# Performance work log

Hardware: AMD Instinct MI355X
Metric: run time of the kernel (lower is better)

Reference implementation:

```python
import jax, jax.numpy as jnp
import numpy as np

NUM_EXPERTS = 8
TOP_K = 2
ROUTE_SCALE = 1.0
DIM = 1024
HID = 1024
B, S = 2, 4096


def setup_inputs() -> dict:
    key = jax.random.key(0)
    ks = jax.random.split(key, 9)
    sc = 0.05
    return {
        "x": jax.random.normal(ks[0], (B, S, DIM), dtype=jnp.float32),
        "gate_w": jax.random.normal(ks[1], (NUM_EXPERTS, DIM), dtype=jnp.float32) * sc,
        "w1": jax.random.normal(ks[2], (NUM_EXPERTS, HID, DIM), dtype=jnp.float32) * sc,
        "w2": jax.random.normal(ks[3], (NUM_EXPERTS, DIM, HID), dtype=jnp.float32) * sc,
        "w3": jax.random.normal(ks[4], (NUM_EXPERTS, HID, DIM), dtype=jnp.float32) * sc,
        "sw1": jax.random.normal(ks[5], (HID, DIM), dtype=jnp.float32) * sc,
        "sw2": jax.random.normal(ks[6], (DIM, HID), dtype=jnp.float32) * sc,
        "sw3": jax.random.normal(ks[7], (HID, DIM), dtype=jnp.float32) * sc,
        "expert_bias": jnp.zeros((NUM_EXPERTS,), dtype=jnp.float32),
    }


def reference(x, gate_w, w1, w2, w3, sw1, sw2, sw3, expert_bias):
    bs, slen, dim = x.shape
    xf = x.reshape(-1, dim)                      # [T, D]

    # ---- router (sigmoid scoring, top-k over scores + bias, gather true scores) ----
    scores = jax.nn.sigmoid((xf @ gate_w.T).astype(jnp.float32))   # [T, E]
    _, sel = jax.lax.top_k(scores + expert_bias[None, :], TOP_K)    # [T, K] int32
    top_scores = jnp.take_along_axis(scores, sel, axis=1) * ROUTE_SCALE  # [T, K]

    # ---- stable sort token-slots by chosen expert (dispatch permutation) ----
    flat_sel = sel.reshape(-1)                       # [T*K]
    order = jnp.argsort(flat_sel, stable=True)       # [T*K]
    scores_sorted = top_scores.reshape(-1)[order]    # [T*K]
    tok_idx = order // TOP_K                         # source token per slot
    expert_ids = flat_sel[order]                     # sorted expert id per slot

    routed = xf[tok_idx]                             # gather [T*K, D]
    # score_before_experts=True: scale inputs by routing score
    routed = (routed.astype(jnp.float32) * scores_sorted[:, None]).astype(x.dtype)

    # ---- grouped expert GLU MLP (loop over fixed expert count, masked) ----
    out_r = jnp.zeros_like(routed)
    for e in range(NUM_EXPERTS):
        m = (expert_ids == e)[:, None]
        h = jax.nn.silu(routed @ w1[e].T) * (routed @ w3[e].T)   # [T*K, H]
        out_r = out_r + jnp.where(m, h @ w2[e].T, jnp.zeros((), routed.dtype))

    # ---- shared expert on all tokens ----
    shared = (jax.nn.silu(xf @ sw1.T) * (xf @ sw3.T)) @ sw2.T    # [T, D]

    # NOTE: original code multiplies by routing scores again after experts
    # (in addition to score_before_experts) -- replicated faithfully.
    out_r = (out_r.astype(jnp.float32) * scores_sorted[:, None]).astype(x.dtype)

    out = shared.at[tok_idx].add(out_r)              # scatter-add combine
    return out.reshape(bs, slen, dim)
```

## Files before the change

### kernel.cpp

```cpp
#include <hip/hip_runtime.h>
#include <stdint.h>

typedef unsigned short u16;
typedef unsigned int u32;

#define T_TOK 8192
#define DIMSZ 1024
#define HIDSZ 1024
#define NE 8
#define NSLOT (T_TOK * 2)
#define NPAD (NSLOT + 1024)

typedef __attribute__((ext_vector_type(8))) __bf16 bf16x8;
typedef __attribute__((ext_vector_type(16))) float f32x16;

#define MFMA32(a, b, c) __builtin_amdgcn_mfma_f32_32x32x16_bf16(a, b, c, 0, 0, 0)

__device__ __forceinline__ size_t ablk(int pos, int c) {
  return ((((size_t)(pos >> 7) * 32 + (c >> 5)) * 4 + ((c >> 3) & 3)) * 128 +
          (pos & 127)) * 8 + (c & 7);
}

__device__ __forceinline__ u16 f2bf(float f) {
  u32 u = __builtin_bit_cast(u32, f);
  u += 0x7FFFu + ((u >> 16) & 1u);
  return (u16)(u >> 16);
}
__device__ __forceinline__ float bflo(u32 v) { return __builtin_bit_cast(float, v << 16); }
__device__ __forceinline__ float bfhi(u32 v) { return __builtin_bit_cast(float, v & 0xffff0000u); }
__device__ __forceinline__ u32 pack2(float a, float b) {
  return (u32)f2bf(a) | ((u32)f2bf(b) << 16);
}
__device__ __forceinline__ float silu_f(float v) { return v / (1.f + expf(-v)); }

__global__ __launch_bounds__(256) void convert_blocked(
    const float* __restrict__ s0, const float* __restrict__ s1,
    const float* __restrict__ s2, const float* __restrict__ ss0,
    const float* __restrict__ ss1, const float* __restrict__ ss2,
    u16* __restrict__ d0, u16* __restrict__ d1, u16* __restrict__ d2,
    u16* __restrict__ ds0, u16* __restrict__ ds1, u16* __restrict__ ds2) {
  __shared__ u16 lt[2048];
  int t = blockIdx.x;
  const float* s;
  u16* d;
  if (t < NE * 16 * 32) {
    s = (blockIdx.y == 0) ? s0 : (blockIdx.y == 1) ? s1 : s2;
    d = (blockIdx.y == 0) ? d0 : (blockIdx.y == 1) ? d1 : d2;
  } else {
    t -= NE * 16 * 32;
    s = (blockIdx.y == 0) ? ss0 : (blockIdx.y == 1) ? ss1 : ss2;
    d = (blockIdx.y == 0) ? ds0 : (blockIdx.y == 1) ? ds1 : ds2;
  }
  int rt = t >> 5, kt = t & 31;
  const float* sp = s + (size_t)rt * 64 * 1024 + kt * 32;
  int nl = threadIdx.x >> 2, k0 = (threadIdx.x & 3) * 8;
  float4 a = *(const float4*)(sp + (size_t)nl * 1024 + k0);
  float4 b = *(const float4*)(sp + (size_t)nl * 1024 + k0 + 4);
  uint4 p;
  p.x = pack2(a.x, a.y); p.y = pack2(a.z, a.w);
  p.z = pack2(b.x, b.y); p.w = pack2(b.z, b.w);
  *(uint4*)&lt[(threadIdx.x & 3) * 512 + nl * 8] = p;
  __syncthreads();
  *(uint4*)(d + (size_t)t * 2048 + threadIdx.x * 8) = *(const uint4*)&lt[threadIdx.x * 8];
}

__global__ __launch_bounds__(256) void router_kernel(
    const float* __restrict__ x, const float* __restrict__ gw,
    const float* __restrict__ bias, int* __restrict__ sel,
    float* __restrict__ selscore, u16* __restrict__ xb) {
  int t = blockIdx.x * 4 + (threadIdx.x >> 6);
  int lane = threadIdx.x & 63;
  float a[NE];
#pragma unroll
  for (int e = 0; e < NE; e++) a[e] = 0.f;
#pragma unroll
  for (int j = 0; j < 4; j++) {
    int c = j * 256 + lane * 4;
    float4 xv = *(const float4*)&x[(size_t)t * DIMSZ + c];
    uint2 p;
    p.x = pack2(xv.x, xv.y);
    p.y = pack2(xv.z, xv.w);
    *(uint2*)&xb[ablk(t, c)] = p;
#pragma unroll
    for (int e = 0; e < NE; e++) {
      float4 gv = *(const float4*)&gw[e * DIMSZ + c];
      a[e] = fmaf(xv.x, gv.x, fmaf(xv.y, gv.y, fmaf(xv.z, gv.z, fmaf(xv.w, gv.w, a[e]))));
    }
  }
#pragma unroll
  for (int off = 1; off < 64; off <<= 1)
#pragma unroll
    for (int e = 0; e < NE; e++) a[e] += __shfl_xor(a[e], off);
  if (lane == 0) {
    float s[NE], b[NE];
#pragma unroll
    for (int e = 0; e < NE; e++) {
      s[e] = 1.f / (1.f + expf(-a[e]));
      b[e] = s[e] + bias[e];
    }
    int e1 = 0; float v1 = b[0];
#pragma unroll
    for (int e = 1; e < NE; e++) if (b[e] > v1) { v1 = b[e]; e1 = e; }
    int e2 = -1; float v2 = -1e30f;
#pragma unroll
    for (int e = 0; e < NE; e++) if (e != e1 && b[e] > v2) { v2 = b[e]; e2 = e; }
    sel[t * 2] = e1; sel[t * 2 + 1] = e2;
    selscore[t * 2] = s[e1];
    selscore[t * 2 + 1] = s[e2];
  }
}

__global__ __launch_bounds__(1024) void rank_kernel(
    const int* __restrict__ sel, const float* __restrict__ selscore,
    int* __restrict__ slot2pos, float* __restrict__ slot_score,
    int* __restrict__ counts, int* __restrict__ offsets) {
  __shared__ int hist[NE * 1024];
  __shared__ int tot[NE];
  __shared__ int offs[NE];
  int tid = threadIdx.x;
  int sl[16];
  int h[NE];
#pragma unroll
  for (int e = 0; e < NE; e++) h[e] = 0;
#pragma unroll
  for (int j = 0; j < 4; j++) {
    int4 v = ((const int4*)sel)[tid * 4 + j];
    sl[j * 4 + 0] = v.x; sl[j * 4 + 1] = v.y;
    sl[j * 4 + 2] = v.z; sl[j * 4 + 3] = v.w;
  }
#pragma unroll
  for (int i = 0; i < 16; i++)
#pragma unroll
    for (int e = 0; e < NE; e++) h[e] += (sl[i] == e) ? 1 : 0;
#pragma unroll
  for (int e = 0; e < NE; e++) hist[e * 1024 + tid] = h[e];
  __syncthreads();
  int wid = tid >> 6, lane = tid & 63;
  if (wid < NE) {
    int e = wid;
    int vals[16];
    int lsum = 0;
#pragma unroll
    for (int i = 0; i < 16; i++) {
      int v = hist[e * 1024 + lane * 16 + i];
      vals[i] = lsum;
      lsum += v;
    }
    int incl = lsum;
#pragma unroll
    for (int off = 1; off < 64; off <<= 1) {
      int v = __shfl_up(incl, off);
      if (lane >= off) incl += v;
    }
    int excl = incl - lsum;
#pragma unroll
    for (int i = 0; i < 16; i++) hist[e * 1024 + lane * 16 + i] = vals[i] + excl;
    if (lane == 63) tot[e] = incl;
  }
  __syncthreads();
  if (tid == 0) {
    int acc = 0;
    for (int e = 0; e < NE; e++) {
      offs[e] = acc;
      offsets[e] = acc;
      counts[e] = tot[e];
      acc += (tot[e] + 127) & ~127;
    }
  }
  __syncthreads();
  int base[NE];
#pragma unroll
  for (int e = 0; e < NE; e++) base[e] = offs[e] + hist[e * 1024 + tid];
#pragma unroll
  for (int i = 0; i < 16; i++) {
    int slot = tid * 16 + i;
    int e = sl[i];
    int pos = 0;
#pragma unroll
    for (int k = 0; k < NE; k++) pos += (e == k) ? base[k] : 0;
#pragma unroll
    for (int k = 0; k < NE; k++) base[k] += (e == k) ? 1 : 0;
    slot2pos[slot] = pos;
    slot_score[pos] = selscore[slot];
  }
}

__global__ __launch_bounds__(256) void gather_kernel(
    const float* __restrict__ x, const float* __restrict__ selscore,
    const int* __restrict__ slot2pos, u16* __restrict__ routed) {
  int s = blockIdx.x * 4 + (threadIdx.x >> 6);
  int lane = threadIdx.x & 63;
  int pos = slot2pos[s];
  float sc = selscore[s];
  int t = s >> 1;
#pragma unroll
  for (int j = 0; j < 4; j++) {
    int c = j * 256 + lane * 4;
    float4 v = *(const float4*)&x[(size_t)t * DIMSZ + c];
    uint2 p;
    p.x = pack2(v.x * sc, v.y * sc);
    p.y = pack2(v.z * sc, v.w * sc);
    *(uint2*)&routed[ablk(pos, c)] = p;
  }
}

__global__ __launch_bounds__(256, 3) void dual_glu_gemm(
    const u16* __restrict__ A, const u16* __restrict__ W1,
    const u16* __restrict__ W3, u16* __restrict__ Hout,
    const u16* __restrict__ As, const u16* __restrict__ SW1,
    const u16* __restrict__ SW3, u16* __restrict__ Hs,
    const int* __restrict__ seg_off, const int* __restrict__ seg_cnt) {
  int z = blockIdx.z;
  const u16 *Ap, *w1p, *w3p;
  u16* Hp;
  int soff, scnt;
  if (z < NE) {
    soff = seg_off[z]; scnt = seg_cnt[z];
    Ap = A;
    w1p = W1 + (size_t)z * HIDSZ * DIMSZ;
    w3p = W3 + (size_t)z * HIDSZ * DIMSZ;
    Hp = Hout;
  } else {
    soff = 0; scnt = T_TOK;
    Ap = As; w1p = SW1; w3p = SW3;
    Hp = Hs;
  }
  int mbase = blockIdx.y * 128;
  if (mbase >= scnt) return;
  int nbase = blockIdx.x * 64;

  __shared__ u16 lA[2][4096];
  __shared__ u16 lB1[2][2048];
  __shared__ u16 lB3[2][2048];

  int tid = threadIdx.x;
  int lane = tid & 63;
  int wid = tid >> 6;
  int wy = wid >> 1, wx = wid & 1;
  int l5 = lane >> 5, l31 = lane & 31;
  int aoff = (l5 * 128 + wy * 64 + l31) * 8;
  int boff = (l5 * 64 + wx * 32 + l31) * 8;

  f32x16 acc1[2], acc3[2];
  acc1[0] = (f32x16)0.f; acc1[1] = (f32x16)0.f;
  acc3[0] = (f32x16)0.f; acc3[1] = (f32x16)0.f;

  const u16* gA = Ap + ((size_t)((soff + mbase) >> 7) * 32) * 4096 + tid * 8;
  const u16* gB1 = w1p + ((size_t)(nbase >> 6) * 32) * 2048 + tid * 8;
  const u16* gB3 = w3p + ((size_t)(nbase >> 6) * 32) * 2048 + tid * 8;

  uint4 rA0 = *(const uint4*)gA;
  uint4 rA1 = *(const uint4*)(gA + 2048);
  uint4 rB1 = *(const uint4*)gB1;
  uint4 rB3 = *(const uint4*)gB3;
  gA += 4096; gB1 += 2048; gB3 += 2048;

#define DG_STAGE(B)                                                   \
  *(uint4*)&lA[B][tid * 8] = rA0;                                     \
  *(uint4*)&lA[B][2048 + tid * 8] = rA1;                              \
  *(uint4*)&lB1[B][tid * 8] = rB1;                                    \
  *(uint4*)&lB3[B][tid * 8] = rB3;

#define DG_LOAD()                                                     \
  rA0 = *(const uint4*)gA;                                            \
  rA1 = *(const uint4*)(gA + 2048);                                   \
  rB1 = *(const uint4*)gB1;                                           \
  rB3 = *(const uint4*)gB3;                                           \
  gA += 4096; gB1 += 2048; gB3 += 2048;

#define DG_COMPUTE(B)                                                 \
  _Pragma("unroll")                                                   \
  for (int s = 0; s < 2; s++) {                                       \
    bf16x8 a0 = *(const bf16x8*)&lA[B][aoff + s * 2048];              \
    bf16x8 a1 = *(const bf16x8*)&lA[B][aoff + s * 2048 + 256];        \
    bf16x8 b1 = *(const bf16x8*)&lB1[B][boff + s * 1024];             \
    bf16x8 b3 = *(const bf16x8*)&lB3[B][boff + s * 1024];             \
    acc1[0] = MFMA32(a0, b1, acc1[0]);                                \
    acc3[0] = MFMA32(a0, b3, acc3[0]);                                \
    acc1[1] = MFMA32(a1, b1, acc1[1]);                                \
    acc3[1] = MFMA32(a1, b3, acc3[1]);                                \
  }

  for (int kt = 0; kt < 32; kt += 2) {
    DG_STAGE(0);
    __syncthreads();
    DG_LOAD();
    DG_COMPUTE(0);
    DG_STAGE(1);
    __syncthreads();
    if (kt < 30) { DG_LOAD(); }
    DG_COMPUTE(1);
  }

#pragma unroll
  for (int i = 0; i < 2; i++) {
    int colg = nbase + wx * 32 + l31;
#pragma unroll
    for (int r = 0; r < 16; r++) {
      int rowl = (r & 3) + 8 * (r >> 2) + 4 * l5;
      int grow = mbase + wy * 64 + i * 32 + rowl;
      if (grow < scnt)
        Hp[ablk(soff + grow, colg)] = f2bf(silu_f(acc1[i][r]) * acc3[i][r]);
    }
  }
}

__global__ __launch_bounds__(256, 3) void gemm2_kernel(
    const u16* __restrict__ A, const u16* __restrict__ W, u16* __restrict__ OutB,
    const u16* __restrict__ As, const u16* __restrict__ SW, float* __restrict__ OutF,
    const float* __restrict__ scale, const int* __restrict__ seg_off,
    const int* __restrict__ seg_cnt) {
  int z = blockIdx.z;
  const u16 *Ap, *wp;
  int soff, scnt;
  if (z < NE) {
    soff = seg_off[z]; scnt = seg_cnt[z];
    Ap = A; wp = W + (size_t)z * DIMSZ * HIDSZ;
  } else {
    soff = 0; scnt = T_TOK;
    Ap = As; wp = SW;
  }
  int mbase = blockIdx.y * 128;
  if (mbase >= scnt) return;
  int nbase = blockIdx.x * 128;

  __shared__ u16 lA[2][4096];
  __shared__ u16 lB[2][4096];

  int tid = threadIdx.x;
  int lane = tid & 63;
  int wid = tid >> 6;
  int wy = wid >> 1, wx = wid & 1;
  int l5 = lane >> 5, l31 = lane & 31;
  int aoff = (l5 * 128 + wy * 64 + l31) * 8;
  int boff = wx * 2048 + (l5 * 64 + l31) * 8;

  f32x16 acc[2][2];
  acc[0][0] = (f32x16)0.f; acc[0][1] = (f32x16)0.f;
  acc[1][0] = (f32x16)0.f; acc[1][1] = (f32x16)0.f;

  const u16* gA = Ap + ((size_t)((soff + mbase) >> 7) * 32) * 4096 + tid * 8;
  const u16* gB0 = wp + ((size_t)(nbase >> 6) * 32) * 2048 + tid * 8;
  const u16* gB1 = wp + ((size_t)((nbase >> 6) + 1) * 32) * 2048 + tid * 8;

  uint4 rA0 = *(const uint4*)gA;
  uint4 rA1 = *(const uint4*)(gA + 2048);
  uint4 rB0 = *(const uint4*)gB0;
  uint4 rB1 = *(const uint4*)gB1;
  gA += 4096; gB0 += 2048; gB1 += 2048;

#define G2_STAGE(B)                                                   \
  *(uint4*)&lA[B][tid * 8] = rA0;                                     \
  *(uint4*)&lA[B][2048 + tid * 8] = rA1;                              \
  *(uint4*)&lB[B][tid * 8] = rB0;                                     \
  *(uint4*)&lB[B][2048 + tid * 8] = rB1;

#define G2_LOAD()                                                     \
  rA0 = *(const uint4*)gA;                                            \
  rA1 = *(const uint4*)(gA + 2048);                                   \
  rB0 = *(const uint4*)gB0;                                           \
  rB1 = *(const uint4*)gB1;                                           \
  gA += 4096; gB0 += 2048; gB1 += 2048;

#define G2_COMPUTE(B)                                                 \
  _Pragma("unroll")                                                   \
  for (int s = 0; s < 2; s++) {                                       \
    bf16x8 a0 = *(const bf16x8*)&lA[B][aoff + s * 2048];              \
    bf16x8 a1 = *(const bf16x8*)&lA[B][aoff + s * 2048 + 256];        \
    bf16x8 b0 = *(const bf16x8*)&lB[B][boff + s * 1024];              \
    bf16x8 b1 = *(const bf16x8*)&lB[B][boff + s * 1024 + 256];        \
    acc[0][0] = MFMA32(a0, b0, acc[0][0]);                            \
    acc[0][1] = MFMA32(a0, b1, acc[0][1]);                            \
    acc[1][0] = MFMA32(a1, b0, acc[1][0]);                            \
    acc[1][1] = MFMA32(a1, b1, acc[1][1]);                            \
  }

  for (int kt = 0; kt < 32; kt += 2) {
    G2_STAGE(0);
    __syncthreads();
    G2_LOAD();
    G2_COMPUTE(0);
    G2_STAGE(1);
    __syncthreads();
    if (kt < 30) { G2_LOAD(); }
    G2_COMPUTE(1);
  }

#pragma unroll
  for (int i = 0; i < 2; i++) {
#pragma unroll
    for (int j = 0; j < 2; j++) {
      int colg = nbase + wx * 64 + j * 32 + l31;
#pragma unroll
      for (int r = 0; r < 16; r++) {
        int rowl = (r & 3) + 8 * (r >> 2) + 4 * l5;
        int grow = mbase + wy * 64 + i * 32 + rowl;
        if (grow < scnt) {
          size_t idx = (size_t)(soff + grow) * DIMSZ + colg;
          if (z < NE) {
            OutB[idx] = f2bf(acc[i][j][r] * scale[soff + grow]);
          } else {
            OutF[idx] = acc[i][j][r];
          }
        }
      }
    }
  }
}

__global__ __launch_bounds__(256) void combine_kernel(
    float* __restrict__ out, const u16* __restrict__ Orb,
    const int* __restrict__ slot2pos) {
  int t = blockIdx.x;
  int d = threadIdx.x * 4;
  int p0 = slot2pos[t * 2];
  int p1 = slot2pos[t * 2 + 1];
  float4 o = *(float4*)&out[(size_t)t * DIMSZ + d];
  uint2 a = *(const uint2*)&Orb[(size_t)p0 * DIMSZ + d];
  uint2 b = *(const uint2*)&Orb[(size_t)p1 * DIMSZ + d];
  o.x += bflo(a.x) + bflo(b.x);
  o.y += bfhi(a.x) + bfhi(b.x);
  o.z += bflo(a.y) + bflo(b.y);
  o.w += bfhi(a.y) + bfhi(b.y);
  *(float4*)&out[(size_t)t * DIMSZ + d] = o;
}

extern "C" void kernel_launch(void* const* d_in, const int* in_sizes, int n_in,
                              void* d_out, int out_size, void* d_ws, size_t ws_size,
                              hipStream_t stream) {
  const float* x = (const float*)d_in[0];
  const float* gw = (const float*)d_in[1];
  const float* w1 = (const float*)d_in[2];
  const float* w2 = (const float*)d_in[3];
  const float* w3 = (const float*)d_in[4];
  const float* sw1 = (const float*)d_in[5];
  const float* sw2 = (const float*)d_in[6];
  const float* sw3 = (const float*)d_in[7];
  const float* bias = (const float*)d_in[8];
  float* out = (float*)d_out;

  uint8_t* ws = (uint8_t*)d_ws;
  size_t off = 0;
  auto alloc = [&](size_t b) { size_t o = off; off += (b + 255) & ~(size_t)255; return o; };

  size_t ctrl = alloc(256);
  int* counts = (int*)(ws + ctrl);
  int* offsets = counts + 16;
  int* sel = (int*)(ws + alloc((size_t)NSLOT * 4));
  float* selscore = (float*)(ws + alloc((size_t)NSLOT * 4));
  float* slot_score = (float*)(ws + alloc((size_t)NPAD * 4));
  int* slot2pos = (int*)(ws + alloc((size_t)NSLOT * 4));
  u16* xb = (u16*)(ws + alloc((size_t)T_TOK * DIMSZ * 2));
  u16* routed = (u16*)(ws + alloc((size_t)NPAD * DIMSZ * 2));
  u16* Hbuf = (u16*)(ws + alloc((size_t)NPAD * HIDSZ * 2));
  u16* Orb = (u16*)(ws + alloc((size_t)NPAD * DIMSZ * 2));
  u16* Hs = (u16*)(ws + alloc((size_t)T_TOK * HIDSZ * 2));
  u16* w1b = (u16*)(ws + alloc((size_t)NE * HIDSZ * DIMSZ * 2));
  u16* w2b = (u16*)(ws + alloc((size_t)NE * DIMSZ * HIDSZ * 2));
  u16* w3b = (u16*)(ws + alloc((size_t)NE * HIDSZ * DIMSZ * 2));
  u16* sw1b = (u16*)(ws + alloc((size_t)HIDSZ * DIMSZ * 2));
  u16* sw2b = (u16*)(ws + alloc((size_t)DIMSZ * HIDSZ * 2));
  u16* sw3b = (u16*)(ws + alloc((size_t)HIDSZ * DIMSZ * 2));

  convert_blocked<<<dim3((NE + 1) * 16 * 32, 3), 256, 0, stream>>>(
      w1, w2, w3, sw1, sw2, sw3, w1b, w2b, w3b, sw1b, sw2b, sw3b);

  router_kernel<<<T_TOK / 4, 256, 0, stream>>>(x, gw, bias, sel, selscore, xb);
  rank_kernel<<<1, 1024, 0, stream>>>(sel, selscore, slot2pos, slot_score,
                                      counts, offsets);
  gather_kernel<<<NSLOT / 4, 256, 0, stream>>>(x, selscore, slot2pos, routed);

  dual_glu_gemm<<<dim3(16, 64, NE + 1), 256, 0, stream>>>(
      routed, w1b, w3b, Hbuf, xb, sw1b, sw3b, Hs, offsets, counts);
  gemm2_kernel<<<dim3(8, 64, NE + 1), 256, 0, stream>>>(
      Hbuf, w2b, Orb, Hs, sw2b, out, slot_score, offsets, counts);

  combine_kernel<<<T_TOK, 256, 0, stream>>>(out, Orb, slot2pos);
}
```

Baseline: 496.3 us.

## Use direct global-to-LDS loads with triple-buffered pipeline and larger M tiles

Both expert GEMMs now load tiles straight from global memory into LDS with global_load_lds into a three-stage ring buffer, and wait on vmcnt plus a barrier instead of staging through registers. M tiles grow from 128 to 256 rows, halving the grid in y. The dual GLU GEMM now splits w1 and w3 across the two wave columns and exchanges partial results through LDS for the SiLU product. The gather also reads the already-converted bf16 x instead of fp32 x. The aim is to hide load latency and raise MFMA reuse per tile, at the cost of lower occupancy (launch bound 2), more LDS, and an extra LDS round-trip in the epilogue.

```diff
diff --git a/kernel.cpp b/kernel.cpp
--- a/kernel.cpp
+++ b/kernel.cpp
@@ -32,6 +32,14 @@
   return (u32)f2bf(a) | ((u32)f2bf(b) << 16);
 }
 __device__ __forceinline__ float silu_f(float v) { return v / (1.f + expf(-v)); }
+
+__device__ __forceinline__ void gload16(const void* g, void* l) {
+  __builtin_amdgcn_global_load_lds(
+      (const __attribute__((address_space(1))) unsigned int*)g,
+      (__attribute__((address_space(3))) unsigned int*)l, 16, 0, 0);
+}
+
+#define PIPE_SYNC(N) asm volatile("s_waitcnt vmcnt(" #N ")\n\ts_barrier" ::: "memory")
 
 __global__ __launch_bounds__(256) void convert_blocked(
     const float* __restrict__ s0, const float* __restrict__ s1,
@@ -186,7 +194,7 @@
 }
 
 __global__ __launch_bounds__(256) void gather_kernel(
-    const float* __restrict__ x, const float* __restrict__ selscore,
+    const u16* __restrict__ xb, const float* __restrict__ selscore,
     const int* __restrict__ slot2pos, u16* __restrict__ routed) {
   int s = blockIdx.x * 4 + (threadIdx.x >> 6);
   int lane = threadIdx.x & 63;
@@ -196,15 +204,63 @@
 #pragma unroll
   for (int j = 0; j < 4; j++) {
     int c = j * 256 + lane * 4;
-    float4 v = *(const float4*)&x[(size_t)t * DIMSZ + c];
+    uint2 v = *(const uint2*)&xb[ablk(t, c)];
     uint2 p;
-    p.x = pack2(v.x * sc, v.y * sc);
-    p.y = pack2(v.z * sc, v.w * sc);
+    p.x = pack2(bflo(v.x) * sc, bfhi(v.x) * sc);
+    p.y = pack2(bflo(v.y) * sc, bfhi(v.y) * sc);
     *(uint2*)&routed[ablk(pos, c)] = p;
   }
 }
 
-__global__ __launch_bounds__(256, 3) void dual_glu_gemm(
+
+#define BUFE 12288
+
+#define PIPE_STAGE(B, KT, pA, pB0, pB1)                        \
+  do {                                                         \
+    u16* Lb = &lds[(B) * BUFE];                                \
+    const u16* a_ = (pA) + (size_t)(KT) * 4096;                \
+    gload16(a_, Lb + tid * 8);                                 \
+    gload16(a_ + 2048, Lb + 2048 + tid * 8);                   \
+    gload16(a_ + 32 * 4096, Lb + 4096 + tid * 8);              \
+    gload16(a_ + 32 * 4096 + 2048, Lb + 6144 + tid * 8);       \
+    gload16((pB0) + (size_t)(KT) * 2048, Lb + 8192 + tid * 8); \
+    gload16((pB1) + (size_t)(KT) * 2048, Lb + 10240 + tid * 8);\
+  } while (0)
+
+#define PIPE_COMPUTE(B)                                             \
+  do {                                                              \
+    const u16* La = &lds[(B) * BUFE] + wy * 4096;                   \
+    const u16* Lw = &lds[(B) * BUFE] + 8192 + wx * 2048;            \
+    _Pragma("unroll")                                               \
+    for (int s = 0; s < 2; s++) {                                   \
+      int kc = 2 * s + l5;                                          \
+      bf16x8 b0 = *(const bf16x8*)&Lw[(kc * 64 + l31) * 8];         \
+      bf16x8 b1 = *(const bf16x8*)&Lw[(kc * 64 + 32 + l31) * 8];    \
+      _Pragma("unroll")                                             \
+      for (int i = 0; i < 4; i++) {                                 \
+        bf16x8 a = *(const bf16x8*)&La[(kc * 128 + i * 32 + l31) * 8]; \
+        acc[i][0] = MFMA32(a, b0, acc[i][0]);                       \
+        acc[i][1] = MFMA32(a, b1, acc[i][1]);                       \
+      }                                                             \
+    }                                                               \
+  } while (0)
+
+#define PIPE_LOOP(pA, pB0, pB1)                 \
+  PIPE_STAGE(0, 0, pA, pB0, pB1);               \
+  PIPE_STAGE(1, 1, pA, pB0, pB1);               \
+  {                                             \
+    int c0 = 0, c1 = 1, c2 = 2;                 \
+    for (int kt = 0; kt < 31; ++kt) {           \
+      PIPE_SYNC(6);                             \
+      if (kt < 30) PIPE_STAGE(c2, kt + 2, pA, pB0, pB1); \
+      PIPE_COMPUTE(c0);                         \
+      int tmp = c0; c0 = c1; c1 = c2; c2 = tmp; \
+    }                                           \
+    PIPE_SYNC(0);                               \
+    PIPE_COMPUTE(c0);                           \
+  }
+
+__global__ __launch_bounds__(256, 2) void dual_glu_gemm(
     const u16* __restrict__ A, const u16* __restrict__ W1,
     const u16* __restrict__ W3, u16* __restrict__ Hout,
     const u16* __restrict__ As, const u16* __restrict__ SW1,
@@ -225,87 +281,61 @@
     Ap = As; w1p = SW1; w3p = SW3;
     Hp = Hs;
   }
-  int mbase = blockIdx.y * 128;
+  int mbase = blockIdx.y * 256;
   if (mbase >= scnt) return;
-  int nbase = blockIdx.x * 64;
-
-  __shared__ u16 lA[2][4096];
-  __shared__ u16 lB1[2][2048];
-  __shared__ u16 lB3[2][2048];
+  int hx = blockIdx.x;
+
+  __shared__ u16 lds[3 * BUFE];
 
   int tid = threadIdx.x;
   int lane = tid & 63;
   int wid = tid >> 6;
   int wy = wid >> 1, wx = wid & 1;
   int l5 = lane >> 5, l31 = lane & 31;
-  int aoff = (l5 * 128 + wy * 64 + l31) * 8;
-  int boff = (l5 * 64 + wx * 32 + l31) * 8;
-
-  f32x16 acc1[2], acc3[2];
-  acc1[0] = (f32x16)0.f; acc1[1] = (f32x16)0.f;
-  acc3[0] = (f32x16)0.f; acc3[1] = (f32x16)0.f;
-
-  const u16* gA = Ap + ((size_t)((soff + mbase) >> 7) * 32) * 4096 + tid * 8;
-  const u16* gB1 = w1p + ((size_t)(nbase >> 6) * 32) * 2048 + tid * 8;
-  const u16* gB3 = w3p + ((size_t)(nbase >> 6) * 32) * 2048 + tid * 8;
-
-  uint4 rA0 = *(const uint4*)gA;
-  uint4 rA1 = *(const uint4*)(gA + 2048);
-  uint4 rB1 = *(const uint4*)gB1;
-  uint4 rB3 = *(const uint4*)gB3;
-  gA += 4096; gB1 += 2048; gB3 += 2048;
-
-#define DG_STAGE(B)                                                   \
-  *(uint4*)&lA[B][tid * 8] = rA0;                                     \
-  *(uint4*)&lA[B][2048 + tid * 8] = rA1;                              \
-  *(uint4*)&lB1[B][tid * 8] = rB1;                                    \
-  *(uint4*)&lB3[B][tid * 8] = rB3;
-
-#define DG_LOAD()                                                     \
-  rA0 = *(const uint4*)gA;                                            \
-  rA1 = *(const uint4*)(gA + 2048);                                   \
-  rB1 = *(const uint4*)gB1;                                           \
-  rB3 = *(const uint4*)gB3;                                           \
-  gA += 4096; gB1 += 2048; gB3 += 2048;
-
-#define DG_COMPUTE(B)                                                 \
-  _Pragma("unroll")                                                   \
-  for (int s = 0; s < 2; s++) {                                       \
-    bf16x8 a0 = *(const bf16x8*)&lA[B][aoff + s * 2048];              \
-    bf16x8 a1 = *(const bf16x8*)&lA[B][aoff + s * 2048 + 256];        \
-    bf16x8 b1 = *(const bf16x8*)&lB1[B][boff + s * 1024];             \
-    bf16x8 b3 = *(const bf16x8*)&lB3[B][boff + s * 1024];             \
-    acc1[0] = MFMA32(a0, b1, acc1[0]);                                \
-    acc3[0] = MFMA32(a0, b3, acc3[0]);                                \
-    acc1[1] = MFMA32(a1, b1, acc1[1]);                                \
-    acc3[1] = MFMA32(a1, b3, acc3[1]);                                \
-  }
-
-  for (int kt = 0; kt < 32; kt += 2) {
-    DG_STAGE(0);
-    __syncthreads();
-    DG_LOAD();
-    DG_COMPUTE(0);
-    DG_STAGE(1);
-    __syncthreads();
-    if (kt < 30) { DG_LOAD(); }
-    DG_COMPUTE(1);
-  }
-
-#pragma unroll
-  for (int i = 0; i < 2; i++) {
-    int colg = nbase + wx * 32 + l31;
-#pragma unroll
-    for (int r = 0; r < 16; r++) {
-      int rowl = (r & 3) + 8 * (r >> 2) + 4 * l5;
-      int grow = mbase + wy * 64 + i * 32 + rowl;
-      if (grow < scnt)
-        Hp[ablk(soff + grow, colg)] = f2bf(silu_f(acc1[i][r]) * acc3[i][r]);
-    }
-  }
-}
-
-__global__ __launch_bounds__(256, 3) void gemm2_kernel(
+
+  const u16* pA = Ap + ((size_t)((soff + mbase) >> 7) * 32) * 4096 + tid * 8;
+  const u16* pB1 = w1p + ((size_t)hx * 32) * 2048 + tid * 8;
+  const u16* pB3 = w3p + ((size_t)hx * 32) * 2048 + tid * 8;
+
+  f32x16 acc[4][2];
+#pragma unroll
+  for (int i = 0; i < 4; i++) { acc[i][0] = (f32x16)0.f; acc[i][1] = (f32x16)0.f; }
+
+  PIPE_LOOP(pA, pB1, pB3);
+
+  __syncthreads();
+  float* ex = (float*)lds;
+  if (wx == 0) {
+#pragma unroll
+    for (int i = 0; i < 4; i++)
+#pragma unroll
+      for (int j = 0; j < 2; j++)
+#pragma unroll
+        for (int r = 0; r < 16; r++) {
+          int row = wy * 128 + i * 32 + (r & 3) + 8 * (r >> 2) + 4 * l5;
+          ex[row * 64 + j * 32 + l31] = acc[i][j][r];
+        }
+  }
+  __syncthreads();
+  if (wx == 1) {
+#pragma unroll
+    for (int i = 0; i < 4; i++)
+#pragma unroll
+      for (int j = 0; j < 2; j++)
+#pragma unroll
+        for (int r = 0; r < 16; r++) {
+          int row = wy * 128 + i * 32 + (r & 3) + 8 * (r >> 2) + 4 * l5;
+          int grow = mbase + row;
+          if (grow < scnt) {
+            float h1 = ex[row * 64 + j * 32 + l31];
+            Hp[ablk(soff + grow, hx * 64 + j * 32 + l31)] =
+                f2bf(silu_f(h1) * acc[i][j][r]);
+          }
+        }
+  }
+}
+
+__global__ __launch_bounds__(256, 2) void gemm2_kernel(
     const u16* __restrict__ A, const u16* __restrict__ W, u16* __restrict__ OutB,
     const u16* __restrict__ As, const u16* __restrict__ SW, float* __restrict__ OutF,
     const float* __restrict__ scale, const int* __restrict__ seg_off,
@@ -320,81 +350,37 @@
     soff = 0; scnt = T_TOK;
     Ap = As; wp = SW;
   }
-  int mbase = blockIdx.y * 128;
+  int mbase = blockIdx.y * 256;
   if (mbase >= scnt) return;
   int nbase = blockIdx.x * 128;
 
-  __shared__ u16 lA[2][4096];
-  __shared__ u16 lB[2][4096];
+  __shared__ u16 lds[3 * BUFE];
 
   int tid = threadIdx.x;
   int lane = tid & 63;
   int wid = tid >> 6;
   int wy = wid >> 1, wx = wid & 1;
   int l5 = lane >> 5, l31 = lane & 31;
-  int aoff = (l5 * 128 + wy * 64 + l31) * 8;
-  int boff = wx * 2048 + (l5 * 64 + l31) * 8;
-
-  f32x16 acc[2][2];
-  acc[0][0] = (f32x16)0.f; acc[0][1] = (f32x16)0.f;
-  acc[1][0] = (f32x16)0.f; acc[1][1] = (f32x16)0.f;
-
-  const u16* gA = Ap + ((size_t)((soff + mbase) >> 7) * 32) * 4096 + tid * 8;
-  const u16* gB0 = wp + ((size_t)(nbase >> 6) * 32) * 2048 + tid * 8;
-  const u16* gB1 = wp + ((size_t)((nbase >> 6) + 1) * 32) * 2048 + tid * 8;
-
-  uint4 rA0 = *(const uint4*)gA;
-  uint4 rA1 = *(const uint4*)(gA + 2048);
-  uint4 rB0 = *(const uint4*)gB0;
-  uint4 rB1 = *(const uint4*)gB1;
-  gA += 4096; gB0 += 2048; gB1 += 2048;
-
-#define G2_STAGE(B)                                                   \
-  *(uint4*)&lA[B][tid * 8] = rA0;                                     \
-  *(uint4*)&lA[B][2048 + tid * 8] = rA1;                              \
-  *(uint4*)&lB[B][tid * 8] = rB0;                                     \
-  *(uint4*)&lB[B][2048 + tid * 8] = rB1;
-
-#define G2_LOAD()                                                     \
-  rA0 = *(const uint4*)gA;                                            \
-  rA1 = *(const uint4*)(gA + 2048);                                   \
-  rB0 = *(const uint4*)gB0;                                           \
-  rB1 = *(const uint4*)gB1;                                           \
-  gA += 4096; gB0 += 2048; gB1 += 2048;
-
-#define G2_COMPUTE(B)                                                 \
-  _Pragma("unroll")                                                   \
-  for (int s = 0; s < 2; s++) {                                       \
-    bf16x8 a0 = *(const bf16x8*)&lA[B][aoff + s * 2048];              \
-    bf16x8 a1 = *(const bf16x8*)&lA[B][aoff + s * 2048 + 256];        \
-    bf16x8 b0 = *(const bf16x8*)&lB[B][boff + s * 1024];              \
-    bf16x8 b1 = *(const bf16x8*)&lB[B][boff + s * 1024 + 256];        \
-    acc[0][0] = MFMA32(a0, b0, acc[0][0]);                            \
-    acc[0][1] = MFMA32(a0, b1, acc[0][1]);                            \
-    acc[1][0] = MFMA32(a1, b0, acc[1][0]);                            \
-    acc[1][1] = MFMA32(a1, b1, acc[1][1]);                            \
-  }
-
-  for (int kt = 0; kt < 32; kt += 2) {
-    G2_STAGE(0);
-    __syncthreads();
-    G2_LOAD();
-    G2_COMPUTE(0);
-    G2_STAGE(1);
-    __syncthreads();
-    if (kt < 30) { G2_LOAD(); }
-    G2_COMPUTE(1);
-  }
-
-#pragma unroll
-  for (int i = 0; i < 2; i++) {
+
+  const u16* pA = Ap + ((size_t)((soff + mbase) >> 7) * 32) * 4096 + tid * 8;
+  const u16* pB0 = wp + ((size_t)(nbase >> 6) * 32) * 2048 + tid * 8;
+  const u16* pB1 = pB0 + (size_t)32 * 2048;
+
+  f32x16 acc[4][2];
+#pragma unroll
+  for (int i = 0; i < 4; i++) { acc[i][0] = (f32x16)0.f; acc[i][1] = (f32x16)0.f; }
+
+  PIPE_LOOP(pA, pB0, pB1);
+
+#pragma unroll
+  for (int i = 0; i < 4; i++)
 #pragma unroll
     for (int j = 0; j < 2; j++) {
       int colg = nbase + wx * 64 + j * 32 + l31;
 #pragma unroll
       for (int r = 0; r < 16; r++) {
         int rowl = (r & 3) + 8 * (r >> 2) + 4 * l5;
-        int grow = mbase + wy * 64 + i * 32 + rowl;
+        int grow = mbase + wy * 128 + i * 32 + rowl;
         if (grow < scnt) {
           size_t idx = (size_t)(soff + grow) * DIMSZ + colg;
           if (z < NE) {
@@ -405,7 +391,6 @@
         }
       }
     }
-  }
 }
 
 __global__ __launch_bounds__(256) void combine_kernel(
@@ -468,11 +453,11 @@
   router_kernel<<<T_TOK / 4, 256, 0, stream>>>(x, gw, bias, sel, selscore, xb);
   rank_kernel<<<1, 1024, 0, stream>>>(sel, selscore, slot2pos, slot_score,
                                       counts, offsets);
-  gather_kernel<<<NSLOT / 4, 256, 0, stream>>>(x, selscore, slot2pos, routed);
-
-  dual_glu_gemm<<<dim3(16, 64, NE + 1), 256, 0, stream>>>(
+  gather_kernel<<<NSLOT / 4, 256, 0, stream>>>(xb, selscore, slot2pos, routed);
+
+  dual_glu_gemm<<<dim3(16, 32, NE + 1), 256, 0, stream>>>(
       routed, w1b, w3b, Hbuf, xb, sw1b, sw3b, Hs, offsets, counts);
-  gemm2_kernel<<<dim3(8, 64, NE + 1), 256, 0, stream>>>(
+  gemm2_kernel<<<dim3(8, 32, NE + 1), 256, 0, stream>>>(
       Hbuf, w2b, Orb, Hs, sw2b, out, slot_score, offsets, counts);
 
   combine_kernel<<<T_TOK, 256, 0, stream>>>(out, Orb, slot2pos);
```

New measurement: 534.2 us. 1.08x slower.
